# Kernel tuning notes

Hardware: AMD Instinct MI355X
Metric: run time of the kernel (lower is better)

The kernel has to match this reference:

```python
import jax, jax.numpy as jnp
import numpy as np

NUM_TOKENS, TOKEN_DIM, NUM_HEADS, REF_DIM = 10, 96, 4, 96


def setup_inputs() -> dict:
    key = jax.random.key(0)
    k0, k1, k2, k3, k4 = jax.random.split(key, 5)
    ref_emb = jax.random.normal(k0, (32, 2048, REF_DIM), dtype=jnp.float32)
    tokens = jax.random.normal(k1, (NUM_TOKENS, TOKEN_DIM), dtype=jnp.float32)
    # nn.Linear weights are [out, in]; forward computes x @ W.T
    Wq = jax.random.normal(k2, (TOKEN_DIM, REF_DIM), dtype=jnp.float32) * (1.0 / np.sqrt(REF_DIM))
    Wk = jax.random.normal(k3, (TOKEN_DIM, TOKEN_DIM), dtype=jnp.float32) * (1.0 / np.sqrt(TOKEN_DIM))
    Wv = jax.random.normal(k4, (NUM_HEADS, TOKEN_DIM), dtype=jnp.float32) * (1.0 / np.sqrt(TOKEN_DIM))
    return {"ref_emb": ref_emb, "tokens": tokens, "Wq": Wq, "Wk": Wk, "Wv": Wv}


def reference(ref_emb, tokens, Wq, Wk, Wv):
    # k: (N, D) tanh'd projected tokens
    k = jnp.tanh(tokens @ Wk.T)
    # q: (B, T, D)
    q = jnp.tanh(ref_emb @ Wq.T)
    # additive attention scores: s (B, T, N, D)
    s = jnp.tanh(q[:, :, None, :] + k[None, None, :, :])
    # logits: (B, T, N, H)
    logits = jnp.einsum('btnd,hd->btnh', s, Wv)
    attn = jax.nn.softmax(logits, axis=2)  # softmax over tokens
    # style: (B, T, D, H) -> mean over heads -> (B, T, D)
    style = jnp.einsum('btnh,nd->btdh', attn, tokens).mean(axis=-1)
    return style
```

## Files before the change

### kernel.cpp

```cpp
#include <hip/hip_runtime.h>
#include <rocwmma/rocwmma.hpp>
#include <cstddef>

#define NT 10
#define TD 96
#define NH 4
#define NPOS (32 * 2048)
#define TPB 256
#define PPB 32
#define LDQ 104

#define WS_WQ 0
#define WS_KV2 18432
#define WS_WVP 23040
#define WS_C 23808
#define WS_BYTES 23824

typedef _Float16 h2 __attribute__((ext_vector_type(2)));

__device__ __forceinline__ h2 pack_h2(float a, float b) {
    return __builtin_bit_cast(h2, __builtin_amdgcn_cvt_pkrtz(a, b));
}

__device__ __forceinline__ float fast_tanh(float x) {
    float e = __expf(2.0f * x);
    return 1.0f - 2.0f * __builtin_amdgcn_rcpf(e + 1.0f);
}

__device__ __forceinline__ float dot2acc(h2 a, h2 b, float c) {
#if __has_builtin(__builtin_amdgcn_fdot2)
    return __builtin_amdgcn_fdot2(a, b, c, false);
#else
    c = fmaf((float)a[0], (float)b[0], c);
    return fmaf((float)a[1], (float)b[1], c);
#endif
}

__global__ __launch_bounds__(256) void gst_prep(
    const float* __restrict__ tokens,
    const float* __restrict__ Wq,
    const float* __restrict__ Wk,
    const float* __restrict__ Wv,
    char* __restrict__ ws)
{
    h2* wqH = (h2*)(ws + WS_WQ);
    float* kv2 = (float*)(ws + WS_KV2);
    h2* wvp = (h2*)(ws + WS_WVP);
    float* Cws = (float*)(ws + WS_C);
    const int b = blockIdx.x;
    const int tid = threadIdx.x;

    if (tid < 2 * (TD / 2)) {
        int r = 2 * b + tid / (TD / 2);
        int c = tid % (TD / 2);
        float2 f = ((const float2*)(Wq + r * TD))[c];
        wqH[r * (TD / 2) + c] = pack_h2(f.x, f.y);
    }
    if (tid < 2 * NT) {
        int d = 2 * b + tid / NT;
        int n = tid % NT;
        const float4* tr = (const float4*)(tokens + n * TD);
        const float4* wr = (const float4*)(Wk + d * TD);
        float acc = 0.0f;
        #pragma unroll
        for (int j = 0; j < TD / 4; ++j) {
            float4 a = tr[j];
            float4 w = wr[j];
            acc = fmaf(a.x, w.x, acc);
            acc = fmaf(a.y, w.y, acc);
            acc = fmaf(a.z, w.z, acc);
            acc = fmaf(a.w, w.w, acc);
        }
        kv2[d * 12 + n] = __expf(2.0f * fast_tanh(acc));
    }
    if (tid < 2 * 2) {
        int d = 2 * b + (tid >> 1);
        kv2[d * 12 + 10 + (tid & 1)] = 0.0f;
    }
    if (b == 0 && tid < 192) {
        int pp = tid >> 5;
        int l = (tid >> 2) & 7;
        int h = tid & 3;
        wvp[(pp * 8 + l) * 4 + h] =
            pack_h2(Wv[h * TD + 16 * pp + l], Wv[h * TD + 16 * pp + 8 + l]);
    }
    if (b == 0 && tid >= 224 && tid < 224 + NH) {
        int h = tid - 224;
        float c = 0.0f;
        for (int d = 0; d < TD; ++d) c += Wv[h * TD + d];
        Cws[h] = c;
    }
}

__global__ __launch_bounds__(TPB, 6) void gst_main(
    const float* __restrict__ ref_emb,
    const float* __restrict__ tokens,
    const char* __restrict__ ws,
    float* __restrict__ out)
{
    __shared__ __align__(16) _Float16 xS[PPB * LDQ];
    __shared__ __align__(16) _Float16 eqS[PPB * LDQ];
    __shared__ __align__(16) float kvS[TD * 12];
    __shared__ __align__(16) h2 wvpS[6 * 8 * 4];

    const int tid = threadIdx.x;
    const int P0 = blockIdx.x * PPB;

    {
        const float4* src = (const float4*)(ref_emb + (size_t)P0 * TD);
        #pragma unroll
        for (int it = 0; it < 3; ++it) {
            int t = tid + it * TPB;
            int row = t / (TD / 4);
            int c4 = t - row * (TD / 4);
            float4 v = src[t];
            h2* dst = (h2*)(xS + row * LDQ + c4 * 4);
            dst[0] = pack_h2(v.x, v.y);
            dst[1] = pack_h2(v.z, v.w);
        }
        const float4* sKV = (const float4*)(ws + WS_KV2);
        float4* dKV = (float4*)kvS;
        dKV[tid % 288] = sKV[tid % 288];
        if (tid < 32) dKV[256 + tid] = sKV[256 + tid];
        const float4* sWV = (const float4*)(ws + WS_WVP);
        float4* dWV = (float4*)wvpS;
        if (tid >= 64 && tid < 112) dWV[tid - 64] = sWV[tid - 64];
    }
    __syncthreads();

    {
        using namespace rocwmma;
        const int lane = tid & 63;
        const int wid = tid >> 6;
        const int ph = wid >> 1;
        const int dh = wid & 1;
        const int arow = lane & 15;
        const int kgrp = lane >> 4;

        fragment<matrix_a, 16, 16, 16, float16_t, row_major> fa[6];
        #pragma unroll
        for (int kb = 0; kb < 6; ++kb)
            load_matrix_sync(fa[kb],
                (const float16_t*)(xS + ph * 16 * LDQ + kb * 16), LDQ);

        const float16_t* wq16 = (const float16_t*)(ws + WS_WQ);
        fragment<accumulator, 16, 16, 16, float> fc[3];
        #pragma unroll
        for (int t = 0; t < 3; ++t) {
            fill_fragment(fc[t], 0.0f);
            #pragma unroll
            for (int kb = 0; kb < 6; ++kb) {
                fragment<matrix_b, 16, 16, 16, float16_t, col_major> fb;
                load_matrix_sync(fb, wq16 + (dh * 3 + t) * 16 * TD + kb * 16, TD);
                mma_sync(fc[t], fa[kb], fb, fc[t]);
            }
        }
        #pragma unroll
        for (int t = 0; t < 3; ++t) {
            const int d = dh * 48 + t * 16 + arow;
            #pragma unroll
            for (int e = 0; e < 4; ++e) {
                const int p = ph * 16 + kgrp * 4 + e;
                eqS[p * LDQ + d] = (_Float16)__expf(2.0f * fast_tanh(fc[t].x[e]));
            }
        }
    }
    __syncthreads();

    const int prow = tid >> 3;
    const int pos = P0 + prow;
    const int l = tid & 7;
    const _Float16* eqrow = eqS + prow * LDQ;

    float R[NT][NH];
    #pragma unroll
    for (int n = 0; n < NT; ++n)
        #pragma unroll
        for (int h = 0; h < NH; ++h) R[n][h] = 0.0f;

    #pragma unroll
    for (int pp = 0; pp < 6; ++pp) {
        const int d1 = 16 * pp + l;
        const float Eq1 = (float)eqrow[d1];
        const float Eq2 = (float)eqrow[d1 + 8];

        const float* r1 = kvS + d1 * 12;
        const float* r2 = kvS + (d1 + 8) * 12;
        const float4 ka1 = *(const float4*)(r1);
        const float4 kb1 = *(const float4*)(r1 + 4);
        const float2 kc1 = *(const float2*)(r1 + 8);
        const float4 ka2 = *(const float4*)(r2);
        const float4 kb2 = *(const float4*)(r2 + 4);
        const float2 kc2 = *(const float2*)(r2 + 8);
        const float ek1[NT] = {ka1.x, ka1.y, ka1.z, ka1.w, kb1.x, kb1.y, kb1.z, kb1.w, kc1.x, kc1.y};
        const float ek2[NT] = {ka2.x, ka2.y, ka2.z, ka2.w, kb2.x, kb2.y, kb2.z, kb2.w, kc2.x, kc2.y};

        const h2* wrow = &wvpS[(pp * 8 + l) * 4];
        const h2 w0 = wrow[0], w1 = wrow[1], w2 = wrow[2], w3 = wrow[3];

        #pragma unroll
        for (int n = 0; n < NT; ++n) {
            float v1 = __builtin_amdgcn_rcpf(fmaf(Eq1, ek1[n], 1.0f));
            float v2 = __builtin_amdgcn_rcpf(fmaf(Eq2, ek2[n], 1.0f));
            h2 rp = pack_h2(v1, v2);
            R[n][0] = dot2acc(rp, w0, R[n][0]);
            R[n][1] = dot2acc(rp, w1, R[n][1]);
            R[n][2] = dot2acc(rp, w2, R[n][2]);
            R[n][3] = dot2acc(rp, w3, R[n][3]);
        }
    }

    const bool myb0 = (l & 1) != 0;
    const bool myb1 = (l & 2) != 0;
    float lh[NT];
    #pragma unroll
    for (int n = 0; n < NT; ++n) {
        float L0 = R[n][0], L1 = R[n][1];
        float L2 = R[n][2], L3 = R[n][3];
        L0 += __shfl_xor(L0, 4);
        L1 += __shfl_xor(L1, 4);
        L2 += __shfl_xor(L2, 4);
        L3 += __shfl_xor(L3, 4);
        float m0 = myb1 ? L2 : L0, m1 = myb1 ? L3 : L1;
        float t0 = myb1 ? L0 : L2, t1 = myb1 ? L1 : L3;
        m0 += __shfl_xor(t0, 2);
        m1 += __shfl_xor(t1, 2);
        float mm = myb0 ? m1 : m0, tt = myb0 ? m0 : m1;
        lh[n] = mm + __shfl_xor(tt, 1);
    }

    {
        const float4 Call = *(const float4*)(ws + WS_C);
        const float Ch = myb0 ? (myb1 ? Call.w : Call.y)
                              : (myb1 ? Call.z : Call.x);
        #pragma unroll
        for (int n = 0; n < NT; ++n) lh[n] = fmaf(-2.0f, lh[n], Ch);
    }

    float m = lh[0];
    #pragma unroll
    for (int n = 1; n < NT; ++n) m = fmaxf(m, lh[n]);
    float e[NT];
    float ssum = 0.0f;
    #pragma unroll
    for (int n = 0; n < NT; ++n) {
        e[n] = __expf(lh[n] - m);
        ssum += e[n];
    }
    const float inv = 0.25f * __builtin_amdgcn_rcpf(ssum);
    float wn[NT];
    #pragma unroll
    for (int n = 0; n < NT; ++n) {
        float v = e[n] * inv;
        v += __shfl_xor(v, 1);
        v += __shfl_xor(v, 2);
        wn[n] = v;
    }

    float4* ob = (float4*)(out + (size_t)pos * TD);
    const float4* t4 = (const float4*)tokens;
    #pragma unroll
    for (int jj = 0; jj < 3; ++jj) {
        const int d4 = l + 8 * jj;
        float4 o = make_float4(0.f, 0.f, 0.f, 0.f);
        #pragma unroll
        for (int n = 0; n < NT; ++n) {
            float4 t = t4[n * (TD / 4) + d4];
            o.x = fmaf(wn[n], t.x, o.x);
            o.y = fmaf(wn[n], t.y, o.y);
            o.z = fmaf(wn[n], t.z, o.z);
            o.w = fmaf(wn[n], t.w, o.w);
        }
        ob[d4] = o;
    }
}

extern "C" void kernel_launch(void* const* d_in, const int* in_sizes, int n_in,
                              void* d_out, int out_size, void* d_ws, size_t ws_size,
                              hipStream_t stream) {
    const float* ref_emb = (const float*)d_in[0];
    const float* tokens  = (const float*)d_in[1];
    const float* Wq      = (const float*)d_in[2];
    const float* Wk      = (const float*)d_in[3];
    const float* Wv      = (const float*)d_in[4];
    float* out = (float*)d_out;

    gst_prep<<<48, 256, 0, stream>>>(tokens, Wq, Wk, Wv, (char*)d_ws);
    gst_main<<<NPOS / PPB, TPB, 0, stream>>>(ref_emb, tokens,
                                             (const char*)d_ws, out);
}
```

Baseline: 38.85 us.

## Give each wavefront its own position slice and drop the block barrier

Each wavefront now loads and converts its own 8 positions, runs the WMMA projection over all 96 output columns, and writes the exp(2·tanh) result in place into its own shared-memory slice. This removes the separate eq buffer and the second block-wide __syncthreads. Token embeddings are also staged in LDS instead of being read from global memory in the output loop. In exchange, each wave computes 16-row MMA tiles where only 8 rows are kept, so MMA work doubles. The unused rows read neighbouring slices, and for the last wave memory past the buffer, but those results are discarded.

```diff
diff --git a/kernel.cpp b/kernel.cpp
--- a/kernel.cpp
+++ b/kernel.cpp
@@ -98,79 +98,87 @@
     const char* __restrict__ ws,
     float* __restrict__ out)
 {
-    __shared__ __align__(16) _Float16 xS[PPB * LDQ];
-    __shared__ __align__(16) _Float16 eqS[PPB * LDQ];
+    __shared__ __align__(16) _Float16 xS[4 * 8 * LDQ];
     __shared__ __align__(16) float kvS[TD * 12];
     __shared__ __align__(16) h2 wvpS[6 * 8 * 4];
+    __shared__ __align__(16) float tokS[NT * TD];
 
     const int tid = threadIdx.x;
-    const int P0 = blockIdx.x * PPB;
-
-    {
-        const float4* src = (const float4*)(ref_emb + (size_t)P0 * TD);
-        #pragma unroll
-        for (int it = 0; it < 3; ++it) {
-            int t = tid + it * TPB;
-            int row = t / (TD / 4);
-            int c4 = t - row * (TD / 4);
-            float4 v = src[t];
-            h2* dst = (h2*)(xS + row * LDQ + c4 * 4);
+    const int lane = tid & 63;
+    const int wid = tid >> 6;
+    const int posbase = blockIdx.x * PPB + wid * 8;
+    _Float16* slice = xS + wid * 8 * LDQ;
+
+    {
+        const float4* src = (const float4*)(ref_emb + (size_t)posbase * TD);
+        #pragma unroll
+        for (int j = 0; j < 3; ++j) {
+            int idx = lane + 64 * j;
+            int row = idx / 24;
+            int c4 = idx - row * 24;
+            float4 v = src[idx];
+            h2* dst = (h2*)(slice + row * LDQ + c4 * 4);
             dst[0] = pack_h2(v.x, v.y);
             dst[1] = pack_h2(v.z, v.w);
         }
+    }
+    {
         const float4* sKV = (const float4*)(ws + WS_KV2);
         float4* dKV = (float4*)kvS;
-        dKV[tid % 288] = sKV[tid % 288];
+        dKV[tid] = sKV[tid];
         if (tid < 32) dKV[256 + tid] = sKV[256 + tid];
         const float4* sWV = (const float4*)(ws + WS_WVP);
         float4* dWV = (float4*)wvpS;
-        if (tid >= 64 && tid < 112) dWV[tid - 64] = sWV[tid - 64];
+        if (tid < 48) dWV[tid] = sWV[tid];
+        if (tid < NT * TD / 4)
+            ((float4*)tokS)[tid] = ((const float4*)tokens)[tid];
     }
     __syncthreads();
 
     {
         using namespace rocwmma;
-        const int lane = tid & 63;
-        const int wid = tid >> 6;
-        const int ph = wid >> 1;
-        const int dh = wid & 1;
         const int arow = lane & 15;
         const int kgrp = lane >> 4;
 
         fragment<matrix_a, 16, 16, 16, float16_t, row_major> fa[6];
         #pragma unroll
         for (int kb = 0; kb < 6; ++kb)
-            load_matrix_sync(fa[kb],
-                (const float16_t*)(xS + ph * 16 * LDQ + kb * 16), LDQ);
+            load_matrix_sync(fa[kb], (const float16_t*)(slice + kb * 16), LDQ);
 
         const float16_t* wq16 = (const float16_t*)(ws + WS_WQ);
-        fragment<accumulator, 16, 16, 16, float> fc[3];
-        #pragma unroll
-        for (int t = 0; t < 3; ++t) {
-            fill_fragment(fc[t], 0.0f);
+        #pragma unroll
+        for (int pass = 0; pass < 2; ++pass) {
+            fragment<accumulator, 16, 16, 16, float> fc[3];
             #pragma unroll
-            for (int kb = 0; kb < 6; ++kb) {
-                fragment<matrix_b, 16, 16, 16, float16_t, col_major> fb;
-                load_matrix_sync(fb, wq16 + (dh * 3 + t) * 16 * TD + kb * 16, TD);
-                mma_sync(fc[t], fa[kb], fb, fc[t]);
+            for (int t = 0; t < 3; ++t) {
+                fill_fragment(fc[t], 0.0f);
+                #pragma unroll
+                for (int kb = 0; kb < 6; ++kb) {
+                    fragment<matrix_b, 16, 16, 16, float16_t, col_major> fb;
+                    load_matrix_sync(fb,
+                        wq16 + (pass * 3 + t) * 16 * TD + kb * 16, TD);
+                    mma_sync(fc[t], fa[kb], fb, fc[t]);
+                }
             }
-        }
-        #pragma unroll
-        for (int t = 0; t < 3; ++t) {
-            const int d = dh * 48 + t * 16 + arow;
-            #pragma unroll
-            for (int e = 0; e < 4; ++e) {
-                const int p = ph * 16 + kgrp * 4 + e;
-                eqS[p * LDQ + d] = (_Float16)__expf(2.0f * fast_tanh(fc[t].x[e]));
+            if (kgrp < 2) {
+                #pragma unroll
+                for (int t = 0; t < 3; ++t) {
+                    const int d = pass * 48 + t * 16 + arow;
+                    #pragma unroll
+                    for (int e = 0; e < 4; ++e) {
+                        const int p = kgrp * 4 + e;
+                        slice[p * LDQ + d] =
+                            (_Float16)__expf(2.0f * fast_tanh(fc[t].x[e]));
+                    }
+                }
             }
         }
     }
-    __syncthreads();
-
-    const int prow = tid >> 3;
-    const int pos = P0 + prow;
-    const int l = tid & 7;
-    const _Float16* eqrow = eqS + prow * LDQ;
+
+    const int prow = lane >> 3;
+    const int pos = posbase + prow;
+    const int l = lane & 7;
+    const _Float16* eqrow = slice + prow * LDQ;
 
     float R[NT][NH];
     #pragma unroll
@@ -258,7 +266,7 @@
     }
 
     float4* ob = (float4*)(out + (size_t)pos * TD);
-    const float4* t4 = (const float4*)tokens;
+    const float4* t4 = (const float4*)tokS;
     #pragma unroll
     for (int jj = 0; jj < 3; ++jj) {
         const int d4 = l + 8 * jj;
```

After: 41.55 us. +6.9%, slower.
